# Kernel tuning notes

Hardware: AMD Instinct MI355X
Metric: run time of the kernel (lower is better)

## Reference

```python
import jax, jax.numpy as jnp
import numpy as np

B, DETER, STOCH, ACT_DIM, HIDDEN, BLOCKS, DEMB = 4096, 4096, 1024, 32, 512, 8, 16
EPS = 1e-4
OUT_B = DETER // BLOCKS            # 512 per-block output
IN_B0 = 4 * HIDDEN + OUT_B          # 2560 per-block input of first hidden block-GEMM


def rmsnorm(x, g):
    return x * jax.lax.rsqrt(jnp.mean(x * x, axis=-1, keepdims=True) + EPS) * g


def setup_inputs() -> dict:
    key = jax.random.key(0)
    ks = jax.random.split(key, 16)
    n = lambda k, s: (jax.random.normal(k, s, jnp.float32) * 0.02)
    return {
        'stoch': jax.random.normal(ks[0], (B, STOCH), jnp.float32),
        'deter': jax.random.normal(ks[1], (B, DETER), jnp.float32),
        'action': jax.random.normal(ks[2], (B, ACT_DIM), jnp.float32),
        'd_emb': jax.random.normal(ks[3], (B, DEMB), jnp.float32),
        # four input branches: Linear -> RMSNorm -> SiLU
        'W0': n(ks[4], (DETER, HIDDEN)), 'b0': jnp.zeros(HIDDEN), 'g0': jnp.ones(HIDDEN),
        'W1': n(ks[5], (STOCH, HIDDEN)), 'b1': jnp.zeros(HIDDEN), 'g1': jnp.ones(HIDDEN),
        'W2': n(ks[6], (ACT_DIM, HIDDEN)), 'b2': jnp.zeros(HIDDEN), 'g2': jnp.ones(HIDDEN),
        'W3': n(ks[7], (DEMB, HIDDEN)), 'b3': jnp.zeros(HIDDEN), 'g3': jnp.ones(HIDDEN),
        # block-diagonal hidden layers (dynlayers=2)
        'Wh0': n(ks[8], (BLOCKS, IN_B0, OUT_B)), 'bh0': jnp.zeros(DETER), 'gh0': jnp.ones(DETER),
        'Wh1': n(ks[9], (BLOCKS, OUT_B, OUT_B)), 'bh1': jnp.zeros(DETER), 'gh1': jnp.ones(DETER),
        # block-diagonal GRU gate projection: deter -> 3*deter
        'Wg': n(ks[10], (BLOCKS, OUT_B, 3 * OUT_B)), 'bg': jnp.zeros(3 * DETER),
    }


def reference(stoch, deter, action, d_emb,
              W0, b0, g0, W1, b1, g1, W2, b2, g2, W3, b3, g3,
              Wh0, bh0, gh0, Wh1, bh1, gh1, Wg, bg):
    act = jax.nn.silu
    Bsz = action.shape[0]
    stoch = stoch.reshape(Bsz, -1)
    # action / clip(|action|, min=1).detach()
    action = action / jax.lax.stop_gradient(jnp.maximum(jnp.abs(action), 1.0))

    x0 = act(rmsnorm(deter @ W0 + b0, g0))
    x1 = act(rmsnorm(stoch @ W1 + b1, g1))
    x2 = act(rmsnorm(action @ W2 + b2, g2))
    x3 = act(rmsnorm(d_emb @ W3 + b3, g3))
    x = jnp.concatenate([x0, x1, x2, x3], axis=-1)          # [B, 4H]

    xg = jnp.broadcast_to(x[:, None, :], (Bsz, BLOCKS, 4 * HIDDEN))
    dg = deter.reshape(Bsz, BLOCKS, OUT_B)                   # flat2group(deter)
    h = jnp.concatenate([dg, xg], axis=-1)                   # [B, blocks, in_b0]

    # hidden layer 0: BlockLinear -> RMSNorm(full width) -> act
    h = jnp.einsum('bgi,gio->bgo', h, Wh0).reshape(Bsz, DETER) + bh0
    h = act(rmsnorm(h, gh0))
    # hidden layer 1
    h = jnp.einsum('bgi,gio->bgo', h.reshape(Bsz, BLOCKS, OUT_B), Wh1).reshape(Bsz, DETER) + bh1
    h = act(rmsnorm(h, gh1))

    # GRU gates via block-diagonal GEMM: [B, blocks, 3*out_b]
    gates = jnp.einsum('bgi,gio->bgo', h.reshape(Bsz, BLOCKS, OUT_B), Wg).reshape(Bsz, 3 * DETER) + bg
    gg = gates.reshape(Bsz, BLOCKS, 3 * OUT_B)
    reset = gg[..., :OUT_B].reshape(Bsz, DETER)
    cand = gg[..., OUT_B:2 * OUT_B].reshape(Bsz, DETER)
    update = gg[..., 2 * OUT_B:].reshape(Bsz, DETER)

    reset = jax.nn.sigmoid(reset)
    cand = jnp.tanh(reset * cand)
    update = jax.nn.sigmoid(update - 1.0)
    return update * cand + (1.0 - update) * deter
```

## Files before the change

kernel.cpp:

```cpp
#include <hip/hip_runtime.h>
#include <hip/hip_bf16.h>
#include <cstdint>

typedef __bf16 bf16x8 __attribute__((ext_vector_type(8)));
typedef float f32x4 __attribute__((ext_vector_type(4)));
typedef unsigned short u16x8 __attribute__((ext_vector_type(8)));
typedef unsigned short u16x4 __attribute__((ext_vector_type(4)));

__device__ __forceinline__ unsigned short f2bf(float f) {
  unsigned int u = __float_as_uint(f);
  u += 0x7FFFu + ((u >> 16) & 1u);
  return (unsigned short)(u >> 16);
}
__device__ __forceinline__ float bf2f(unsigned short h) {
  return __uint_as_float(((unsigned int)h) << 16);
}
__device__ __forceinline__ float frcp_(float x) { return __builtin_amdgcn_rcpf(x); }
__device__ __forceinline__ float sigmoid_fast(float x) { return frcp_(1.f + __expf(-x)); }
__device__ __forceinline__ float tanh_fast(float x) { return 1.f - 2.f * frcp_(__expf(2.f * x) + 1.f); }
__device__ __forceinline__ float siluf_(float x) { return x * sigmoid_fast(x); }

#define GLOAD_LDS16(gsrc, ldst) \
  __builtin_amdgcn_global_load_lds((const __attribute__((address_space(1))) void*)(gsrc), \
                                   (__attribute__((address_space(3))) void*)(ldst), 16, 0, 0)

#define S_BARRIER() asm volatile("s_barrier" ::: "memory")
#define LGKM0() asm volatile("s_waitcnt lgkmcnt(0)" ::: "memory")

__device__ __forceinline__ void xcd_tile(int& x, int& y, int& z) {
  const int gx = gridDim.x, gy = gridDim.y;
  const int nwg = gx * gy * gridDim.z;
  const int lin = (blockIdx.z * gy + blockIdx.y) * gx + blockIdx.x;
  const int cpx = nwg >> 3;
  const int t = (lin & 7) * cpx + (lin >> 3);
  x = t % gx;
  const int r = t / gx;
  y = r % gy;
  z = r / gy;
}

template<int F32>
__device__ __forceinline__ void gemm8_core(
    const unsigned short* __restrict__ A1, int lda1, int K1,
    const unsigned short* __restrict__ A2, int lda2, int K2,
    const unsigned short* __restrict__ Bt, int ldb,
    void* __restrict__ C, int ldc,
    int tm, int tn, unsigned short* lds)
{
  const int tid = threadIdx.x;
  const int lane = tid & 63;
  const int wave = tid >> 6;
  const int wm = (wave >> 2) * 128;
  const int wn = (wave & 3) * 64;
  const int frow = lane & 15;
  const int chunk16 = (lane >> 4) * 16;
  const int nt = (K1 + K2) >> 5;

  auto stageA = [&](unsigned short* dstA, int ktBase) {
    const unsigned short* Ab; int alda, kloc;
    if (ktBase >= K1) { Ab = A2; alda = lda2; kloc = ktBase - K1; }
    else              { Ab = A1; alda = lda1; kloc = ktBase; }
#pragma unroll
    for (int j = 0; j < 2; ++j) {
      int o = j * 8192 + tid * 16;
      int so = o ^ (((o >> 7) & 3) << 4);
      int row = so >> 6, cb = so & 63;
      GLOAD_LDS16(Ab + (long long)(tm + row) * alda + kloc + (cb >> 1),
                  (char*)dstA + j * 8192 + wave * 1024);
    }
  };
  auto stageB = [&](unsigned short* dstB, int ktBase) {
#pragma unroll
    for (int j = 0; j < 2; ++j) {
      int o = j * 8192 + tid * 16;
      int so = o ^ (((o >> 7) & 3) << 4);
      int row = so >> 6, cb = so & 63;
      GLOAD_LDS16(Bt + (long long)(tn + row) * ldb + ktBase + (cb >> 1),
                  (char*)dstB + j * 8192 + wave * 1024);
    }
  };
  auto ldswz = [&](const unsigned short* rg, int row) -> bf16x8 {
    int o = row * 64 + chunk16;
    o ^= ((o >> 7) & 3) << 4;
    return *(const bf16x8*)((const char*)rg + o);
  };

  f32x4 acc[8][4] = {};

#pragma unroll
  for (int t = 0; t < 3; ++t) {
    unsigned short* b = lds + t * 16384;
    stageA(b, t * 32); stageB(b + 8192, t * 32);
  }
  asm volatile("s_waitcnt vmcnt(8)" ::: "memory");
  S_BARRIER();

  for (int T = 0; T < nt; ++T) {
    unsigned short* b = lds + (T & 3) * 16384;
    unsigned short* bs = lds + ((T + 3) & 3) * 16384;
    bf16x8 av[4], bv[4];
#pragma unroll
    for (int j = 0; j < 4; ++j) bv[j] = ldswz(b + 8192, wn + j * 16 + frow);
#pragma unroll
    for (int i = 0; i < 4; ++i) av[i] = ldswz(b, wm + i * 16 + frow);
    if (T + 3 < nt) stageA(bs, (T + 3) * 32);
    S_BARRIER();
    LGKM0();
    __builtin_amdgcn_s_setprio(1);
#pragma unroll
    for (int i = 0; i < 4; ++i)
#pragma unroll
      for (int j = 0; j < 4; ++j)
        acc[i][j] = __builtin_amdgcn_mfma_f32_16x16x32_bf16(av[i], bv[j], acc[i][j], 0, 0, 0);
    __builtin_amdgcn_s_setprio(0);
    bf16x8 a2[4];
#pragma unroll
    for (int i = 0; i < 4; ++i) a2[i] = ldswz(b, wm + 64 + i * 16 + frow);
    if (T + 3 < nt) {
      stageB(bs + 8192, (T + 3) * 32);
      asm volatile("s_waitcnt vmcnt(8)" ::: "memory");
    } else if (T + 2 < nt) {
      asm volatile("s_waitcnt vmcnt(4)" ::: "memory");
    } else if (T + 1 < nt) {
      asm volatile("s_waitcnt vmcnt(0)" ::: "memory");
    }
    S_BARRIER();
    LGKM0();
    __builtin_amdgcn_s_setprio(1);
#pragma unroll
    for (int i = 0; i < 4; ++i)
#pragma unroll
      for (int j = 0; j < 4; ++j)
        acc[4 + i][j] = __builtin_amdgcn_mfma_f32_16x16x32_bf16(a2[i], bv[j], acc[4 + i][j], 0, 0, 0);
    __builtin_amdgcn_s_setprio(0);
  }

  const int cr = (lane >> 4) * 4;
  const int cc = lane & 15;
#pragma unroll
  for (int mf = 0; mf < 8; ++mf) {
    const int r0 = tm + wm + mf * 16 + cr;
#pragma unroll
    for (int j = 0; j < 4; ++j) {
      const int col = tn + wn + j * 16 + cc;
#pragma unroll
      for (int i = 0; i < 4; ++i) {
        if (F32) ((float*)C)[(long long)(r0 + i) * ldc + col] = acc[mf][j][i];
        else ((unsigned short*)C)[(long long)(r0 + i) * ldc + col] = f2bf(acc[mf][j][i]);
      }
    }
  }
}

__global__ __launch_bounds__(512, 2) void gemm8(
    const unsigned short* __restrict__ A1, int lda1, long long a1_bs, int K1,
    const unsigned short* __restrict__ A2, int lda2, int K2,
    const unsigned short* __restrict__ Bt, int ldb, long long bt_bs,
    unsigned short* __restrict__ C, int ldc, long long c_bs)
{
  __shared__ unsigned short lds[4 * 16384];
  int tx, ty, g;
  xcd_tile(tx, ty, g);
  gemm8_core<0>(A1 + (long long)g * a1_bs, lda1, K1, A2, lda2, K2,
                Bt + (long long)g * bt_bs, ldb,
                C + (long long)g * c_bs, ldc,
                ty * 256, tx * 256, lds);
}

struct BCfg { const unsigned short* A; int lda; int K;
              const unsigned short* Bt; int ldb; unsigned short* C; };
struct BPack { BCfg c[9]; };
__global__ __launch_bounds__(512, 2) void gemm8_branch(BPack p) {
  __shared__ unsigned short lds[4 * 16384];
  int tx, ty, z;
  xcd_tile(tx, ty, z);
  BCfg c = p.c[z];
  gemm8_core<0>(c.A, c.lda, c.K, nullptr, 0, 0, c.Bt, c.ldb, c.C, 512,
                ty * 256, tx * 256, lds);
}

__global__ __launch_bounds__(512, 2) void gemm_gru(
    const unsigned short* __restrict__ hB,
    const unsigned short* __restrict__ Wgt,
    const float* __restrict__ bg,
    const unsigned short* __restrict__ deterB,
    float* __restrict__ out)
{
  __shared__ unsigned short lds[4 * 14336];
  int txi, tyi, g;
  xcd_tile(txi, tyi, g);
  const int tm = tyi * 256;
  const int tn = txi * 192;
  const unsigned short* A  = hB + g * 512;
  const unsigned short* Bt = Wgt + (long long)g * 1536 * 512;
  const int tid = threadIdx.x, lane = tid & 63, wave = tid >> 6;
  const int wm = (wave >> 2) * 128;
  const int wv = wave & 3;
  const int frow = lane & 15, chunk16 = (lane >> 4) * 16;
  const bool wlow = (wave < 4);
  const int nt = 16;

  auto stageA = [&](unsigned short* buf, int kt) {
#pragma unroll
    for (int j = 0; j < 2; ++j) {
      int o = j * 8192 + tid * 16;
      int so = o ^ (((o >> 7) & 3) << 4);
      int row = so >> 6, cb = so & 63;
      GLOAD_LDS16(A + (long long)(tm + row) * 4096 + kt + (cb >> 1),
                  (char*)buf + j * 8192 + wave * 1024);
    }
  };
  auto stageB = [&](unsigned short* buf, int kt) {
    char* bb = (char*)(buf + 8192);
    {
      int o = tid * 16;
      int so = o ^ (((o >> 7) & 3) << 4);
      int row = so >> 6, cb = so & 63;
      GLOAD_LDS16(Bt + (long long)(tn + row) * 512 + kt + (cb >> 1),
                  bb + wave * 1024);
    }
    if (tid < 256) {
      int o = 8192 + tid * 16;
      int so = o ^ (((o >> 7) & 3) << 4);
      int row = so >> 6, cb = so & 63;
      GLOAD_LDS16(Bt + (long long)(tn + row) * 512 + kt + (cb >> 1),
                  bb + 8192 + wave * 1024);
    }
  };
  auto ldA = [&](const unsigned short* buf, int row) -> bf16x8 {
    int o = row * 64 + chunk16; o ^= ((o >> 7) & 3) << 4;
    return *(const bf16x8*)((const char*)buf + o);
  };
  auto ldB = [&](const unsigned short* buf, int nf) -> bf16x8 {
    int row = wv * 48 + nf * 16 + frow;
    int o = row * 64 + chunk16; o ^= ((o >> 7) & 3) << 4;
    return *(const bf16x8*)((const char*)(buf + 8192) + o);
  };
  auto vm_gate = [&](int n_lo, int n_hi) {
    if (wlow) {
      if (n_lo == 8) asm volatile("s_waitcnt vmcnt(8)" ::: "memory");
      else if (n_lo == 4) asm volatile("s_waitcnt vmcnt(4)" ::: "memory");
      else asm volatile("s_waitcnt vmcnt(0)" ::: "memory");
    } else {
      if (n_hi == 6) asm volatile("s_waitcnt vmcnt(6)" ::: "memory");
      else if (n_hi == 3) asm volatile("s_waitcnt vmcnt(3)" ::: "memory");
      else asm volatile("s_waitcnt vmcnt(0)" ::: "memory");
    }
  };

  f32x4 acc[8][3] = {};

#pragma unroll
  for (int t = 0; t < 3; ++t) {
    unsigned short* b = lds + t * 14336;
    stageA(b, t * 32); stageB(b, t * 32);
  }
  vm_gate(8, 6);
  S_BARRIER();

  for (int T = 0; T < nt; ++T) {
    unsigned short* b = lds + (T & 3) * 14336;
    unsigned short* bs = lds + ((T + 3) & 3) * 14336;
    bf16x8 av[4], bv[3];
#pragma unroll
    for (int j = 0; j < 3; ++j) bv[j] = ldB(b, j);
#pragma unroll
    for (int i = 0; i < 4; ++i) av[i] = ldA(b, wm + i * 16 + frow);
    if (T + 3 < nt) stageA(bs, (T + 3) * 32);
    S_BARRIER();
    LGKM0();
    __builtin_amdgcn_s_setprio(1);
#pragma unroll
    for (int i = 0; i < 4; ++i)
#pragma unroll
      for (int j = 0; j < 3; ++j)
        acc[i][j] = __builtin_amdgcn_mfma_f32_16x16x32_bf16(av[i], bv[j], acc[i][j], 0, 0, 0);
    __builtin_amdgcn_s_setprio(0);
    bf16x8 a2[4];
#pragma unroll
    for (int i = 0; i < 4; ++i) a2[i] = ldA(b, wm + 64 + i * 16 + frow);
    if (T + 3 < nt) {
      stageB(bs, (T + 3) * 32);
      vm_gate(8, 6);
    } else if (T + 2 < nt) {
      vm_gate(4, 3);
    } else if (T + 1 < nt) {
      vm_gate(0, 0);
    }
    S_BARRIER();
    LGKM0();
    __builtin_amdgcn_s_setprio(1);
#pragma unroll
    for (int i = 0; i < 4; ++i)
#pragma unroll
      for (int j = 0; j < 3; ++j)
        acc[4 + i][j] = __builtin_amdgcn_mfma_f32_16x16x32_bf16(a2[i], bv[j], acc[4 + i][j], 0, 0, 0);
    __builtin_amdgcn_s_setprio(0);
  }

  const int cr = (lane >> 4) * 4, cc = lane & 15;
  const int o_col = (txi * 4 + wv) * 16 + cc;
  const int gcol = g * 512 + o_col;
  const float bgr = bg[g * 1536 + o_col];
  const float bgc = bg[g * 1536 + 512 + o_col];
  const float bgu = bg[g * 1536 + 1024 + o_col];
#pragma unroll
  for (int mf = 0; mf < 8; ++mf) {
    const int r0 = tm + wm + mf * 16 + cr;
#pragma unroll
    for (int i = 0; i < 4; ++i) {
      const long long off = (long long)(r0 + i) * 4096 + gcol;
      float dt = bf2f(deterB[off]);
      float reset = sigmoid_fast(acc[mf][0][i] + bgr);
      float cand  = tanh_fast(reset * (acc[mf][1][i] + bgc));
      float upd   = sigmoid_fast(acc[mf][2][i] + bgu - 1.f);
      out[off] = upd * cand + (1.f - upd) * dt;
    }
  }
}

__device__ __forceinline__ void transpose_dev(
    const float* __restrict__ src, unsigned short* __restrict__ dst,
    int R, int C, int bx, int by, int bz, float (*t)[132])
{
  const long long bOff = (long long)bz * R * C;
  src += bOff; dst += bOff;
  const int c0 = bx * 128, r0 = by * 32;
  const int tid = threadIdx.x;
  const int tx = tid & 31, ty = tid >> 5;
#pragma unroll
  for (int j = 0; j < 4; ++j) {
    int row = ty + j * 8;
    float4 v = *(const float4*)&src[(long long)(r0 + row) * C + c0 + tx * 4];
    *(float4*)&t[row][tx * 4] = v;
  }
  __syncthreads();
#pragma unroll
  for (int j = 0; j < 4; ++j) {
    int idx = j * 256 + tid;
    int c = idx >> 3, rg = idx & 7;
    u16x4 o;
    o.x = f2bf(t[rg * 4 + 0][c]); o.y = f2bf(t[rg * 4 + 1][c]);
    o.z = f2bf(t[rg * 4 + 2][c]); o.w = f2bf(t[rg * 4 + 3][c]);
    *(u16x4*)&dst[(long long)(c0 + c) * R + r0 + rg * 4] = o;
  }
}

__device__ __forceinline__ void transpose_wg_dev(
    const float* __restrict__ src, unsigned short* __restrict__ dst,
    int bx, int by, int bz, float (*t)[132])
{
  src += (long long)bz * 512 * 1536;
  dst += (long long)bz * 1536 * 512;
  const int c0 = bx * 128, r0 = by * 32;
  const int tid = threadIdx.x;
  const int tx = tid & 31, ty = tid >> 5;
#pragma unroll
  for (int j = 0; j < 4; ++j) {
    int row = ty + j * 8;
    float4 v = *(const float4*)&src[(long long)(r0 + row) * 1536 + c0 + tx * 4];
    *(float4*)&t[row][tx * 4] = v;
  }
  __syncthreads();
#pragma unroll
  for (int j = 0; j < 4; ++j) {
    int idx = j * 256 + tid;
    int c = idx >> 3, rg = idx & 7;
    int cc = c0 + c;
    int gate = cc >> 9, o = cc & 511;
    int nn = (o >> 4) * 48 + gate * 16 + (o & 15);
    u16x4 oo;
    oo.x = f2bf(t[rg * 4 + 0][c]); oo.y = f2bf(t[rg * 4 + 1][c]);
    oo.z = f2bf(t[rg * 4 + 2][c]); oo.w = f2bf(t[rg * 4 + 3][c]);
    *(u16x4*)&dst[(long long)nn * 512 + r0 + rg * 4] = oo;
  }
}

__global__ __launch_bounds__(256) void preproc_k(
    const float* __restrict__ deter, unsigned short* __restrict__ deterB,
    const float* __restrict__ stoch, unsigned short* __restrict__ stochB,
    const float* __restrict__ W0, unsigned short* __restrict__ W0t,
    const float* __restrict__ W1, unsigned short* __restrict__ W1t,
    const float* __restrict__ Wh0, unsigned short* __restrict__ Wh0t,
    const float* __restrict__ Wh1, unsigned short* __restrict__ Wh1t,
    const float* __restrict__ Wg, unsigned short* __restrict__ Wgt)
{
  __shared__ float t[32][132];
  int b = blockIdx.x;
  if (b < 20480) {
    int i = b * 256 + threadIdx.x;
    const float* s; unsigned short* d;
    if (i < 4194304) { s = deter; d = deterB; }
    else { i -= 4194304; if (i >= 1048576) return; s = stoch; d = stochB; }
    float4 v = ((const float4*)s)[i];
    u16x4 o;
    o.x = f2bf(v.x); o.y = f2bf(v.y); o.z = f2bf(v.z); o.w = f2bf(v.w);
    ((u16x4*)d)[i] = o;
    return;
  }
  b -= 20480;
  if (b < 512)  { transpose_dev(W0, W0t, 4096, 512, b & 3, b >> 2, 0, t); return; }
  b -= 512;
  if (b < 128)  { transpose_dev(W1, W1t, 1024, 512, b & 3, b >> 2, 0, t); return; }
  b -= 128;
  if (b < 2560) { transpose_dev(Wh0, Wh0t, 2560, 512, b & 3, (b >> 2) % 80, b / 320, t); return; }
  b -= 2560;
  if (b < 512)  { transpose_dev(Wh1, Wh1t, 512, 512, b & 3, (b >> 2) & 15, b >> 6, t); return; }
  b -= 512;
  transpose_wg_dev(Wg, Wgt, b % 12, (b / 12) & 15, b / 192, t);
}

__global__ __launch_bounds__(256) void branch_epi_k(
    const unsigned short* __restrict__ yP0b, const unsigned short* __restrict__ yP1b,
    const float* __restrict__ b0, const float* __restrict__ g0,
    const float* __restrict__ b1, const float* __restrict__ g1,
    const float* __restrict__ action, const float* __restrict__ demb,
    const float* __restrict__ W2, const float* __restrict__ b2, const float* __restrict__ g2,
    const float* __restrict__ W3, const float* __restrict__ b3, const float* __restrict__ g3,
    unsigned short* __restrict__ x)
{
  const int row = blockIdx.x, br = blockIdx.y;
  const int tid = threadIdx.x, lane = tid & 63, wave = tid >> 6;
  __shared__ float red[4];
  __shared__ float a[32];
  float v0, v1;
  const float* gg;
  if (br == 0) {
    const unsigned short* p = yP0b + (long long)row * 512;
    v0 = b0[tid]; v1 = b0[tid + 256];
#pragma unroll
    for (int c = 0; c < 8; ++c) {
      v0 += bf2f(p[(long long)c * 2097152 + tid]);
      v1 += bf2f(p[(long long)c * 2097152 + tid + 256]);
    }
    gg = g0;
  } else if (br == 1) {
    const unsigned short* p = yP1b + (long long)row * 512;
    v0 = b1[tid] + bf2f(p[tid]);
    v1 = b1[tid + 256] + bf2f(p[tid + 256]);
    gg = g1;
  } else {
    const int K = (br == 3) ? 16 : 32;
    const float* W  = (br == 3) ? W3 : W2;
    const float* bb = (br == 3) ? b3 : b2;
    gg = (br == 3) ? g3 : g2;
    if (tid < K) {
      float t = (br == 3) ? demb[(long long)row * 16 + tid]
                          : action[(long long)row * 32 + tid];
      if (br == 2) t = t / fmaxf(fabsf(t), 1.f);
      a[tid] = t;
    }
    __syncthreads();
    v0 = bb[tid]; v1 = bb[tid + 256];
    for (int k = 0; k < K; ++k) {
      float av = a[k];
      v0 += av * W[k * 512 + tid];
      v1 += av * W[k * 512 + tid + 256];
    }
  }
  float ss = v0 * v0 + v1 * v1;
  for (int o = 32; o > 0; o >>= 1) ss += __shfl_xor(ss, o);
  if (lane == 0) red[wave] = ss;
  __syncthreads();
  float ms = (red[0] + red[1] + red[2] + red[3]) * (1.f / 512.f);
  float sc = rsqrtf(ms + 1e-4f);
  unsigned short* xr = x + (long long)row * 2048 + br * 512;
  xr[tid]       = f2bf(siluf_(v0 * sc * gg[tid]));
  xr[tid + 256] = f2bf(siluf_(v1 * sc * gg[tid + 256]));
}

__global__ __launch_bounds__(256) void epi_full_k(
    const unsigned short* __restrict__ y, const float* __restrict__ bias,
    const float* __restrict__ gw, unsigned short* __restrict__ h)
{
  const int row = blockIdx.x;
  __shared__ float red[4];
  const int tid = threadIdx.x, lane = tid & 63, wave = tid >> 6;
  const u16x8* yv = (const u16x8*)(y + (long long)row * 4096);
  u16x8 ta = yv[tid], tb = yv[256 + tid];
  float ba[8], bb8[8];
  *(float4*)&ba[0]  = *(const float4*)&bias[tid * 8];
  *(float4*)&ba[4]  = *(const float4*)&bias[tid * 8 + 4];
  *(float4*)&bb8[0] = *(const float4*)&bias[(256 + tid) * 8];
  *(float4*)&bb8[4] = *(const float4*)&bias[(256 + tid) * 8 + 4];
  float fa[8], fb[8];
  float ss = 0.f;
#pragma unroll
  for (int e = 0; e < 8; ++e) {
    fa[e] = bf2f(ta[e]) + ba[e];  ss += fa[e] * fa[e];
    fb[e] = bf2f(tb[e]) + bb8[e]; ss += fb[e] * fb[e];
  }
  for (int o = 32; o > 0; o >>= 1) ss += __shfl_xor(ss, o);
  if (lane == 0) red[wave] = ss;
  __syncthreads();
  float ms = (red[0] + red[1] + red[2] + red[3]) * (1.f / 4096.f);
  float sc = rsqrtf(ms + 1e-4f);
  float ga[8], gb8[8];
  *(float4*)&ga[0]  = *(const float4*)&gw[tid * 8];
  *(float4*)&ga[4]  = *(const float4*)&gw[tid * 8 + 4];
  *(float4*)&gb8[0] = *(const float4*)&gw[(256 + tid) * 8];
  *(float4*)&gb8[4] = *(const float4*)&gw[(256 + tid) * 8 + 4];
  u16x8 oa, ob;
#pragma unroll
  for (int e = 0; e < 8; ++e) {
    oa[e] = f2bf(siluf_(fa[e] * sc * ga[e]));
    ob[e] = f2bf(siluf_(fb[e] * sc * gb8[e]));
  }
  u16x8* hv = (u16x8*)(h + (long long)row * 4096);
  hv[tid] = oa;
  hv[256 + tid] = ob;
}

extern "C" void kernel_launch(void* const* d_in, const int* in_sizes, int n_in,
                              void* d_out, int out_size, void* d_ws, size_t ws_size,
                              hipStream_t stream) {
  const float* stoch  = (const float*)d_in[0];
  const float* deter  = (const float*)d_in[1];
  const float* action = (const float*)d_in[2];
  const float* demb   = (const float*)d_in[3];
  const float* W0 = (const float*)d_in[4];
  const float* b0 = (const float*)d_in[5];
  const float* g0 = (const float*)d_in[6];
  const float* W1 = (const float*)d_in[7];
  const float* b1 = (const float*)d_in[8];
  const float* g1 = (const float*)d_in[9];
  const float* W2 = (const float*)d_in[10];
  const float* b2 = (const float*)d_in[11];
  const float* g2 = (const float*)d_in[12];
  const float* W3 = (const float*)d_in[13];
  const float* b3 = (const float*)d_in[14];
  const float* g3 = (const float*)d_in[15];
  const float* Wh0 = (const float*)d_in[16];
  const float* bh0 = (const float*)d_in[17];
  const float* gh0 = (const float*)d_in[18];
  const float* Wh1 = (const float*)d_in[19];
  const float* bh1 = (const float*)d_in[20];
  const float* gh1 = (const float*)d_in[21];
  const float* Wg  = (const float*)d_in[22];
  const float* bg  = (const float*)d_in[23];
  float* out = (float*)d_out;

  char* ws = (char*)d_ws;
  unsigned short* deterB = (unsigned short*)(ws + 0);
  unsigned short* stochB = (unsigned short*)(ws + 33554432);
  unsigned short* W0t    = (unsigned short*)(ws + 41943040);
  unsigned short* W1t    = (unsigned short*)(ws + 46137344);
  unsigned short* xB     = (unsigned short*)(ws + 47185920);
  unsigned short* yP0b   = (unsigned short*)(ws + 63963136);
  unsigned short* yB     = (unsigned short*)(ws + 63963136);
  unsigned short* yP1b   = (unsigned short*)(ws + 97517568);
  unsigned short* Wh0t   = (unsigned short*)(ws + 105906176);
  unsigned short* Wh1t   = (unsigned short*)(ws + 126877696);
  unsigned short* hB     = (unsigned short*)(ws + 134217728);
  unsigned short* Wgt    = (unsigned short*)(ws + 167772160);
  (void)in_sizes; (void)n_in; (void)out_size; (void)ws_size;

  dim3 b256(256);
  dim3 b512(512);
  preproc_k<<<dim3(25728), b256, 0, stream>>>(deter, deterB, stoch, stochB,
                                              W0, W0t, W1, W1t, Wh0, Wh0t,
                                              Wh1, Wh1t, Wg, Wgt);
  {
    BPack p;
    for (int z = 0; z < 8; ++z)
      p.c[z] = { deterB + z * 512, 4096, 512, W0t + z * 512, 4096,
                 yP0b + (long long)z * 2097152 };
    p.c[8] = { stochB, 1024, 1024, W1t, 1024, yP1b };
    gemm8_branch<<<dim3(2, 16, 9), b512, 0, stream>>>(p);
  }
  branch_epi_k<<<dim3(4096, 4), b256, 0, stream>>>(yP0b, yP1b, b0, g0, b1, g1,
                                                   action, demb, W2, b2, g2, W3, b3, g3, xB);
  gemm8<<<dim3(2, 16, 8), b512, 0, stream>>>(deterB, 4096, 512, 512, xB, 2048, 2048,
                                             Wh0t, 2560, 512LL * 2560, yB, 4096, 512);
  epi_full_k<<<dim3(4096), b256, 0, stream>>>(yB, bh0, gh0, hB);
  gemm8<<<dim3(2, 16, 8), b512, 0, stream>>>(hB, 4096, 512, 512, nullptr, 0, 0,
                                             Wh1t, 512, 512LL * 512, yB, 4096, 512);
  epi_full_k<<<dim3(4096), b256, 0, stream>>>(yB, bh1, gh1, hB);
  gemm_gru<<<dim3(8, 16, 8), b512, 0, stream>>>(hB, Wgt, bg, deterB, out);
}
```

Measured before the change: 327.4 us.

## Switch GEMMs to 256-thread 128x256 tiles with triple-buffered LDS pipeline

Replaces the 512-thread 256x256 GEMM tiles (quad-buffered, prefetch depth 3) with 256-thread 128x256 tiles using a rotating triple buffer with prefetch depth 2, in the generic, branch and GRU GEMMs. The GRU gate kernel gets the same smaller-tile layout with a simpler epilogue over two output sub-blocks. The deter branch split-K is rebalanced from 8 slices to 7 uneven slices so that, with the stoch GEMM, the grid has 8 z-slices, and the epilogue reduction is adjusted to match. The goal is more workgroups and better occupancy and load balance across CUs, at the cost of less operand reuse per tile and a shallower prefetch.

```diff
diff --git a/kernel.cpp b/kernel.cpp
--- a/kernel.cpp
+++ b/kernel.cpp
@@ -40,7 +40,7 @@
 }
 
 template<int F32>
-__device__ __forceinline__ void gemm8_core(
+__device__ __forceinline__ void gemm4_core(
     const unsigned short* __restrict__ A1, int lda1, int K1,
     const unsigned short* __restrict__ A2, int lda2, int K2,
     const unsigned short* __restrict__ Bt, int ldb,
@@ -50,33 +50,34 @@
   const int tid = threadIdx.x;
   const int lane = tid & 63;
   const int wave = tid >> 6;
-  const int wm = (wave >> 2) * 128;
-  const int wn = (wave & 3) * 64;
+  const int wm = (wave >> 1) * 64;
+  const int wn = (wave & 1) * 128;
   const int frow = lane & 15;
   const int chunk16 = (lane >> 4) * 16;
   const int nt = (K1 + K2) >> 5;
 
-  auto stageA = [&](unsigned short* dstA, int ktBase) {
+  auto stageA = [&](unsigned short* buf, int ktBase) {
     const unsigned short* Ab; int alda, kloc;
     if (ktBase >= K1) { Ab = A2; alda = lda2; kloc = ktBase - K1; }
     else              { Ab = A1; alda = lda1; kloc = ktBase; }
 #pragma unroll
     for (int j = 0; j < 2; ++j) {
-      int o = j * 8192 + tid * 16;
+      int o = j * 4096 + tid * 16;
       int so = o ^ (((o >> 7) & 3) << 4);
       int row = so >> 6, cb = so & 63;
       GLOAD_LDS16(Ab + (long long)(tm + row) * alda + kloc + (cb >> 1),
-                  (char*)dstA + j * 8192 + wave * 1024);
-    }
-  };
-  auto stageB = [&](unsigned short* dstB, int ktBase) {
-#pragma unroll
-    for (int j = 0; j < 2; ++j) {
-      int o = j * 8192 + tid * 16;
+                  (char*)buf + j * 4096 + wave * 1024);
+    }
+  };
+  auto stageB = [&](unsigned short* buf, int ktBase) {
+    char* bb = (char*)buf + 8192;
+#pragma unroll
+    for (int j = 0; j < 4; ++j) {
+      int o = j * 4096 + tid * 16;
       int so = o ^ (((o >> 7) & 3) << 4);
       int row = so >> 6, cb = so & 63;
       GLOAD_LDS16(Bt + (long long)(tn + row) * ldb + ktBase + (cb >> 1),
-                  (char*)dstB + j * 8192 + wave * 1024);
+                  bb + j * 4096 + wave * 1024);
     }
   };
   auto ldswz = [&](const unsigned short* rg, int row) -> bf16x8 {
@@ -85,25 +86,24 @@
     return *(const bf16x8*)((const char*)rg + o);
   };
 
-  f32x4 acc[8][4] = {};
-
-#pragma unroll
-  for (int t = 0; t < 3; ++t) {
-    unsigned short* b = lds + t * 16384;
-    stageA(b, t * 32); stageB(b + 8192, t * 32);
-  }
-  asm volatile("s_waitcnt vmcnt(8)" ::: "memory");
+  f32x4 acc[4][8] = {};
+
+  unsigned short* pc = lds;
+  unsigned short* pn = lds + 12288;
+  unsigned short* pf = lds + 24576;
+
+  stageA(pc, 0); stageB(pc, 0);
+  stageA(pn, 32); stageB(pn, 32);
+  asm volatile("s_waitcnt vmcnt(6)" ::: "memory");
   S_BARRIER();
 
   for (int T = 0; T < nt; ++T) {
-    unsigned short* b = lds + (T & 3) * 16384;
-    unsigned short* bs = lds + ((T + 3) & 3) * 16384;
     bf16x8 av[4], bv[4];
 #pragma unroll
-    for (int j = 0; j < 4; ++j) bv[j] = ldswz(b + 8192, wn + j * 16 + frow);
-#pragma unroll
-    for (int i = 0; i < 4; ++i) av[i] = ldswz(b, wm + i * 16 + frow);
-    if (T + 3 < nt) stageA(bs, (T + 3) * 32);
+    for (int i = 0; i < 4; ++i) av[i] = ldswz(pc, wm + i * 16 + frow);
+#pragma unroll
+    for (int j = 0; j < 4; ++j) bv[j] = ldswz(pc + 4096, wn + j * 16 + frow);
+    if (T + 2 < nt) stageA(pf, (T + 2) * 32);
     S_BARRIER();
     LGKM0();
     __builtin_amdgcn_s_setprio(1);
@@ -113,14 +113,12 @@
       for (int j = 0; j < 4; ++j)
         acc[i][j] = __builtin_amdgcn_mfma_f32_16x16x32_bf16(av[i], bv[j], acc[i][j], 0, 0, 0);
     __builtin_amdgcn_s_setprio(0);
-    bf16x8 a2[4];
-#pragma unroll
-    for (int i = 0; i < 4; ++i) a2[i] = ldswz(b, wm + 64 + i * 16 + frow);
-    if (T + 3 < nt) {
-      stageB(bs + 8192, (T + 3) * 32);
-      asm volatile("s_waitcnt vmcnt(8)" ::: "memory");
-    } else if (T + 2 < nt) {
-      asm volatile("s_waitcnt vmcnt(4)" ::: "memory");
+    bf16x8 b2[4];
+#pragma unroll
+    for (int j = 0; j < 4; ++j) b2[j] = ldswz(pc + 4096, wn + 64 + j * 16 + frow);
+    if (T + 2 < nt) {
+      stageB(pf, (T + 2) * 32);
+      if (T + 1 < nt) asm volatile("s_waitcnt vmcnt(6)" ::: "memory");
     } else if (T + 1 < nt) {
       asm volatile("s_waitcnt vmcnt(0)" ::: "memory");
     }
@@ -131,17 +129,18 @@
     for (int i = 0; i < 4; ++i)
 #pragma unroll
       for (int j = 0; j < 4; ++j)
-        acc[4 + i][j] = __builtin_amdgcn_mfma_f32_16x16x32_bf16(a2[i], bv[j], acc[4 + i][j], 0, 0, 0);
+        acc[i][4 + j] = __builtin_amdgcn_mfma_f32_16x16x32_bf16(av[i], b2[j], acc[i][4 + j], 0, 0, 0);
     __builtin_amdgcn_s_setprio(0);
+    unsigned short* t = pc; pc = pn; pn = pf; pf = t;
   }
 
   const int cr = (lane >> 4) * 4;
   const int cc = lane & 15;
 #pragma unroll
-  for (int mf = 0; mf < 8; ++mf) {
+  for (int mf = 0; mf < 4; ++mf) {
     const int r0 = tm + wm + mf * 16 + cr;
 #pragma unroll
-    for (int j = 0; j < 4; ++j) {
+    for (int j = 0; j < 8; ++j) {
       const int col = tn + wn + j * 16 + cc;
 #pragma unroll
       for (int i = 0; i < 4; ++i) {
@@ -152,79 +151,72 @@
   }
 }
 
-__global__ __launch_bounds__(512, 2) void gemm8(
+__global__ __launch_bounds__(256, 2) void gemm4(
     const unsigned short* __restrict__ A1, int lda1, long long a1_bs, int K1,
     const unsigned short* __restrict__ A2, int lda2, int K2,
     const unsigned short* __restrict__ Bt, int ldb, long long bt_bs,
     unsigned short* __restrict__ C, int ldc, long long c_bs)
 {
-  __shared__ unsigned short lds[4 * 16384];
+  __shared__ unsigned short lds[3 * 12288];
   int tx, ty, g;
   xcd_tile(tx, ty, g);
-  gemm8_core<0>(A1 + (long long)g * a1_bs, lda1, K1, A2, lda2, K2,
+  gemm4_core<0>(A1 + (long long)g * a1_bs, lda1, K1, A2, lda2, K2,
                 Bt + (long long)g * bt_bs, ldb,
                 C + (long long)g * c_bs, ldc,
-                ty * 256, tx * 256, lds);
+                ty * 128, tx * 256, lds);
 }
 
 struct BCfg { const unsigned short* A; int lda; int K;
               const unsigned short* Bt; int ldb; unsigned short* C; };
-struct BPack { BCfg c[9]; };
-__global__ __launch_bounds__(512, 2) void gemm8_branch(BPack p) {
-  __shared__ unsigned short lds[4 * 16384];
+struct BPack { BCfg c[8]; };
+__global__ __launch_bounds__(256, 2) void gemm4_branch(BPack p) {
+  __shared__ unsigned short lds[3 * 12288];
   int tx, ty, z;
   xcd_tile(tx, ty, z);
   BCfg c = p.c[z];
-  gemm8_core<0>(c.A, c.lda, c.K, nullptr, 0, 0, c.Bt, c.ldb, c.C, 512,
-                ty * 256, tx * 256, lds);
-}
-
-__global__ __launch_bounds__(512, 2) void gemm_gru(
+  gemm4_core<0>(c.A, c.lda, c.K, nullptr, 0, 0, c.Bt, c.ldb, c.C, 512,
+                ty * 128, tx * 256, lds);
+}
+
+__global__ __launch_bounds__(256, 2) void gemm_gru(
     const unsigned short* __restrict__ hB,
     const unsigned short* __restrict__ Wgt,
     const float* __restrict__ bg,
     const unsigned short* __restrict__ deterB,
     float* __restrict__ out)
 {
-  __shared__ unsigned short lds[4 * 14336];
+  __shared__ unsigned short lds[3 * 10240];
   int txi, tyi, g;
   xcd_tile(txi, tyi, g);
-  const int tm = tyi * 256;
+  const int tm = tyi * 128;
   const int tn = txi * 192;
   const unsigned short* A  = hB + g * 512;
   const unsigned short* Bt = Wgt + (long long)g * 1536 * 512;
   const int tid = threadIdx.x, lane = tid & 63, wave = tid >> 6;
-  const int wm = (wave >> 2) * 128;
-  const int wv = wave & 3;
+  const int wm = (wave >> 1) * 64;
+  const int wn = (wave & 1) * 96;
   const int frow = lane & 15, chunk16 = (lane >> 4) * 16;
-  const bool wlow = (wave < 4);
   const int nt = 16;
 
   auto stageA = [&](unsigned short* buf, int kt) {
 #pragma unroll
     for (int j = 0; j < 2; ++j) {
-      int o = j * 8192 + tid * 16;
+      int o = j * 4096 + tid * 16;
       int so = o ^ (((o >> 7) & 3) << 4);
       int row = so >> 6, cb = so & 63;
       GLOAD_LDS16(A + (long long)(tm + row) * 4096 + kt + (cb >> 1),
-                  (char*)buf + j * 8192 + wave * 1024);
+                  (char*)buf + j * 4096 + wave * 1024);
     }
   };
   auto stageB = [&](unsigned short* buf, int kt) {
-    char* bb = (char*)(buf + 8192);
-    {
-      int o = tid * 16;
+    char* bb = (char*)buf + 8192;
+#pragma unroll
+    for (int j = 0; j < 3; ++j) {
+      int o = j * 4096 + tid * 16;
       int so = o ^ (((o >> 7) & 3) << 4);
       int row = so >> 6, cb = so & 63;
       GLOAD_LDS16(Bt + (long long)(tn + row) * 512 + kt + (cb >> 1),
-                  bb + wave * 1024);
-    }
-    if (tid < 256) {
-      int o = 8192 + tid * 16;
-      int so = o ^ (((o >> 7) & 3) << 4);
-      int row = so >> 6, cb = so & 63;
-      GLOAD_LDS16(Bt + (long long)(tn + row) * 512 + kt + (cb >> 1),
-                  bb + 8192 + wave * 1024);
+                  bb + j * 4096 + wave * 1024);
     }
   };
   auto ldA = [&](const unsigned short* buf, int row) -> bf16x8 {
@@ -232,41 +224,29 @@
     return *(const bf16x8*)((const char*)buf + o);
   };
   auto ldB = [&](const unsigned short* buf, int nf) -> bf16x8 {
-    int row = wv * 48 + nf * 16 + frow;
+    int row = wn + nf * 16 + frow;
     int o = row * 64 + chunk16; o ^= ((o >> 7) & 3) << 4;
-    return *(const bf16x8*)((const char*)(buf + 8192) + o);
-  };
-  auto vm_gate = [&](int n_lo, int n_hi) {
-    if (wlow) {
-      if (n_lo == 8) asm volatile("s_waitcnt vmcnt(8)" ::: "memory");
-      else if (n_lo == 4) asm volatile("s_waitcnt vmcnt(4)" ::: "memory");
-      else asm volatile("s_waitcnt vmcnt(0)" ::: "memory");
-    } else {
-      if (n_hi == 6) asm volatile("s_waitcnt vmcnt(6)" ::: "memory");
-      else if (n_hi == 3) asm volatile("s_waitcnt vmcnt(3)" ::: "memory");
-      else asm volatile("s_waitcnt vmcnt(0)" ::: "memory");
-    }
-  };
-
-  f32x4 acc[8][3] = {};
-
-#pragma unroll
-  for (int t = 0; t < 3; ++t) {
-    unsigned short* b = lds + t * 14336;
-    stageA(b, t * 32); stageB(b, t * 32);
-  }
-  vm_gate(8, 6);
+    return *(const bf16x8*)((const char*)buf + 8192 + o);
+  };
+
+  f32x4 acc[4][6] = {};
+
+  unsigned short* pc = lds;
+  unsigned short* pn = lds + 10240;
+  unsigned short* pf = lds + 20480;
+
+  stageA(pc, 0); stageB(pc, 0);
+  stageA(pn, 32); stageB(pn, 32);
+  asm volatile("s_waitcnt vmcnt(5)" ::: "memory");
   S_BARRIER();
 
   for (int T = 0; T < nt; ++T) {
-    unsigned short* b = lds + (T & 3) * 14336;
-    unsigned short* bs = lds + ((T + 3) & 3) * 14336;
     bf16x8 av[4], bv[3];
 #pragma unroll
-    for (int j = 0; j < 3; ++j) bv[j] = ldB(b, j);
-#pragma unroll
-    for (int i = 0; i < 4; ++i) av[i] = ldA(b, wm + i * 16 + frow);
-    if (T + 3 < nt) stageA(bs, (T + 3) * 32);
+    for (int i = 0; i < 4; ++i) av[i] = ldA(pc, wm + i * 16 + frow);
+#pragma unroll
+    for (int j = 0; j < 3; ++j) bv[j] = ldB(pc, j);
+    if (T + 2 < nt) stageA(pf, (T + 2) * 32);
     S_BARRIER();
     LGKM0();
     __builtin_amdgcn_s_setprio(1);
@@ -276,16 +256,14 @@
       for (int j = 0; j < 3; ++j)
         acc[i][j] = __builtin_amdgcn_mfma_f32_16x16x32_bf16(av[i], bv[j], acc[i][j], 0, 0, 0);
     __builtin_amdgcn_s_setprio(0);
-    bf16x8 a2[4];
-#pragma unroll
-    for (int i = 0; i < 4; ++i) a2[i] = ldA(b, wm + 64 + i * 16 + frow);
-    if (T + 3 < nt) {
-      stageB(bs, (T + 3) * 32);
-      vm_gate(8, 6);
-    } else if (T + 2 < nt) {
-      vm_gate(4, 3);
+    bf16x8 b2[3];
+#pragma unroll
+    for (int j = 0; j < 3; ++j) b2[j] = ldB(pc, 3 + j);
+    if (T + 2 < nt) {
+      stageB(pf, (T + 2) * 32);
+      if (T + 1 < nt) asm volatile("s_waitcnt vmcnt(5)" ::: "memory");
     } else if (T + 1 < nt) {
-      vm_gate(0, 0);
+      asm volatile("s_waitcnt vmcnt(0)" ::: "memory");
     }
     S_BARRIER();
     LGKM0();
@@ -294,27 +272,31 @@
     for (int i = 0; i < 4; ++i)
 #pragma unroll
       for (int j = 0; j < 3; ++j)
-        acc[4 + i][j] = __builtin_amdgcn_mfma_f32_16x16x32_bf16(a2[i], bv[j], acc[4 + i][j], 0, 0, 0);
+        acc[i][3 + j] = __builtin_amdgcn_mfma_f32_16x16x32_bf16(av[i], b2[j], acc[i][3 + j], 0, 0, 0);
     __builtin_amdgcn_s_setprio(0);
+    unsigned short* t = pc; pc = pn; pn = pf; pf = t;
   }
 
   const int cr = (lane >> 4) * 4, cc = lane & 15;
-  const int o_col = (txi * 4 + wv) * 16 + cc;
-  const int gcol = g * 512 + o_col;
-  const float bgr = bg[g * 1536 + o_col];
-  const float bgc = bg[g * 1536 + 512 + o_col];
-  const float bgu = bg[g * 1536 + 1024 + o_col];
-#pragma unroll
-  for (int mf = 0; mf < 8; ++mf) {
-    const int r0 = tm + wm + mf * 16 + cr;
-#pragma unroll
-    for (int i = 0; i < 4; ++i) {
-      const long long off = (long long)(r0 + i) * 4096 + gcol;
-      float dt = bf2f(deterB[off]);
-      float reset = sigmoid_fast(acc[mf][0][i] + bgr);
-      float cand  = tanh_fast(reset * (acc[mf][1][i] + bgc));
-      float upd   = sigmoid_fast(acc[mf][2][i] + bgu - 1.f);
-      out[off] = upd * cand + (1.f - upd) * dt;
+#pragma unroll
+  for (int ob = 0; ob < 2; ++ob) {
+    const int o_col = (txi * 4 + (wave & 1) * 2 + ob) * 16 + cc;
+    const int gcol = g * 512 + o_col;
+    const float bgr = bg[g * 1536 + o_col];
+    const float bgc = bg[g * 1536 + 512 + o_col];
+    const float bgu = bg[g * 1536 + 1024 + o_col];
+#pragma unroll
+    for (int mf = 0; mf < 4; ++mf) {
+      const int r0 = tm + wm + mf * 16 + cr;
+#pragma unroll
+      for (int i = 0; i < 4; ++i) {
+        const long long off = (long long)(r0 + i) * 4096 + gcol;
+        float dt = bf2f(deterB[off]);
+        float reset = sigmoid_fast(acc[mf][ob * 3 + 0][i] + bgr);
+        float cand  = tanh_fast(reset * (acc[mf][ob * 3 + 1][i] + bgc));
+        float upd   = sigmoid_fast(acc[mf][ob * 3 + 2][i] + bgu - 1.f);
+        out[off] = upd * cand + (1.f - upd) * dt;
+      }
     }
   }
 }
@@ -429,7 +411,7 @@
     const unsigned short* p = yP0b + (long long)row * 512;
     v0 = b0[tid]; v1 = b0[tid + 256];
 #pragma unroll
-    for (int c = 0; c < 8; ++c) {
+    for (int c = 0; c < 7; ++c) {
       v0 += bf2f(p[(long long)c * 2097152 + tid]);
       v1 += bf2f(p[(long long)c * 2097152 + tid + 256]);
     }
@@ -556,25 +538,26 @@
   (void)in_sizes; (void)n_in; (void)out_size; (void)ws_size;
 
   dim3 b256(256);
-  dim3 b512(512);
   preproc_k<<<dim3(25728), b256, 0, stream>>>(deter, deterB, stoch, stochB,
                                               W0, W0t, W1, W1t, Wh0, Wh0t,
                                               Wh1, Wh1t, Wg, Wgt);
   {
+    const int k0s[7]  = {0, 640, 1216, 1792, 2368, 2944, 3520};
+    const int klen[7] = {640, 576, 576, 576, 576, 576, 576};
     BPack p;
-    for (int z = 0; z < 8; ++z)
-      p.c[z] = { deterB + z * 512, 4096, 512, W0t + z * 512, 4096,
+    for (int z = 0; z < 7; ++z)
+      p.c[z] = { deterB + k0s[z], 4096, klen[z], W0t + k0s[z], 4096,
                  yP0b + (long long)z * 2097152 };
-    p.c[8] = { stochB, 1024, 1024, W1t, 1024, yP1b };
-    gemm8_branch<<<dim3(2, 16, 9), b512, 0, stream>>>(p);
+    p.c[7] = { stochB, 1024, 1024, W1t, 1024, yP1b };
+    gemm4_branch<<<dim3(2, 32, 8), b256, 0, stream>>>(p);
   }
   branch_epi_k<<<dim3(4096, 4), b256, 0, stream>>>(yP0b, yP1b, b0, g0, b1, g1,
                                                    action, demb, W2, b2, g2, W3, b3, g3, xB);
-  gemm8<<<dim3(2, 16, 8), b512, 0, stream>>>(deterB, 4096, 512, 512, xB, 2048, 2048,
+  gemm4<<<dim3(2, 32, 8), b256, 0, stream>>>(deterB, 4096, 512, 512, xB, 2048, 2048,
                                              Wh0t, 2560, 512LL * 2560, yB, 4096, 512);
   epi_full_k<<<dim3(4096), b256, 0, stream>>>(yB, bh0, gh0, hB);
-  gemm8<<<dim3(2, 16, 8), b512, 0, stream>>>(hB, 4096, 512, 512, nullptr, 0, 0,
+  gemm4<<<dim3(2, 32, 8), b256, 0, stream>>>(hB, 4096, 512, 512, nullptr, 0, 0,
                                              Wh1t, 512, 512LL * 512, yB, 4096, 512);
   epi_full_k<<<dim3(4096), b256, 0, stream>>>(yB, bh1, gh1, hB);
-  gemm_gru<<<dim3(8, 16, 8), b512, 0, stream>>>(hB, Wgt, bg, deterB, out);
-}
+  gemm_gru<<<dim3(8, 32, 8), b256, 0, stream>>>(hB, Wgt, bg, deterB, out);
+}
```

New measurement: 317.3 us (median of 2 runs). 3.1% less time.
